# Kernel tuning notes

Hardware: AMD Instinct MI355X
Metric: run time of the kernel (lower is better)

## Reference

```python
import jax, jax.numpy as jnp
import numpy as np

B, NQ, NKV = 2, 2048, 2048
DIM, CTX_DIM = 1024, 1024
HEADS, DIM_HEAD = 16, 64
INNER = HEADS * DIM_HEAD  # 1024
SCALE = DIM_HEAD ** -0.5


def setup_inputs() -> dict:
    key = jax.random.key(0)
    ks = jax.random.split(key, 6)
    x = jax.random.normal(ks[0], (B, NQ, DIM), dtype=jnp.float32)
    context = jax.random.normal(ks[1], (B, NKV, CTX_DIM), dtype=jnp.float32)
    # nn.Linear weights stored as [out, in] in torch; we keep [in, out] for x @ W.
    Wq = jax.random.normal(ks[2], (DIM, INNER), dtype=jnp.float32) / np.sqrt(DIM)
    Wkv = jax.random.normal(ks[3], (CTX_DIM, 2 * INNER), dtype=jnp.float32) / np.sqrt(CTX_DIM)
    Wout = jax.random.normal(ks[4], (INNER, DIM), dtype=jnp.float32) / np.sqrt(INNER)
    bout = jax.random.normal(ks[5], (DIM,), dtype=jnp.float32) * 0.01
    return {"x": x, "context": context, "Wq": Wq, "Wkv": Wkv, "Wout": Wout, "bout": bout}


def reference(x, context, Wq, Wkv, Wout, bout):
    q = x @ Wq                      # [B, Nq, inner]
    kv = context @ Wkv              # [B, Nkv, 2*inner]
    k, v = jnp.split(kv, 2, axis=-1)

    def split_heads(t):             # [B, N, inner] -> [B, H, N, dh]
        return t.reshape(t.shape[0], t.shape[1], HEADS, DIM_HEAD).transpose(0, 2, 1, 3)

    q, k, v = split_heads(q), split_heads(k), split_heads(v)
    dots = jnp.einsum('bhqd,bhkd->bhqk', q, k) * SCALE  # [B, H, Nq, Nkv]
    attn = jax.nn.softmax(dots, axis=-1)
    out = jnp.einsum('bhqk,bhkd->bhqd', attn, v)        # [B, H, Nq, dh]
    out = out.transpose(0, 2, 1, 3).reshape(out.shape[0], out.shape[2], INNER)
    return out @ Wout + bout        # [B, Nq, dim]
```

## Files before the change

kernel.cpp:

```cpp
#include <hip/hip_runtime.h>
#include <hip/hip_bf16.h>
#include <stdint.h>

#define NQ 2048
#define NKV 2048
#define DIM 1024
#define INNER 1024
#define HEADS 16
#define DH 64
#define BATCH 2

typedef float f32x4 __attribute__((ext_vector_type(4)));
typedef __bf16 bf16x8 __attribute__((ext_vector_type(8)));
typedef unsigned int u32x4 __attribute__((ext_vector_type(4)));

__device__ inline ushort f2b(float f) {
    uint32_t u = __builtin_bit_cast(uint32_t, f);
    u += 0x7fff + ((u >> 16) & 1);
    return (ushort)(u >> 16);
}

__device__ inline uint pkbf16(float lo, float hi) {
    __hip_bfloat162 h = __float22bfloat162_rn(make_float2(lo, hi));
    uint r;
    __builtin_memcpy(&r, &h, 4);
    return r;
}

__device__ __forceinline__ void gload16(const void* g, void* lds) {
    __builtin_amdgcn_global_load_lds(
        (const __attribute__((address_space(1))) unsigned int*)g,
        (__attribute__((address_space(3))) unsigned int*)lds, 16, 0, 0);
}

__global__ void prep(const float* __restrict__ x, const float* __restrict__ ctx,
                     const float* __restrict__ Wq, const float* __restrict__ Wkv,
                     const float* __restrict__ Wout,
                     ushort* __restrict__ xb, ushort* __restrict__ cb,
                     ushort* __restrict__ Wqt, ushort* __restrict__ Wkvt,
                     ushort* __restrict__ Woutt) {
    int z = blockIdx.z;
    if (z < 4) {
        __shared__ ushort tile[32][33];
        const float* src; ushort* dst; int C;
        if (z == 0)      { src = Wq;          dst = Wqt;                C = 1024; }
        else if (z == 1) { src = Wkv;         dst = Wkvt;               C = 2048; }
        else if (z == 2) { src = Wkv + 1024;  dst = Wkvt + 1024 * 1024; C = 2048; }
        else             { src = Wout;        dst = Woutt;              C = 1024; }
        int c0 = blockIdx.x * 32, r0 = blockIdx.y * 32;
        int tx = threadIdx.x, ty = threadIdx.y;
#pragma unroll
        for (int i = 0; i < 4; i++)
            tile[ty + i * 8][tx] = f2b(src[(size_t)(r0 + ty + i * 8) * C + c0 + tx]);
        __syncthreads();
#pragma unroll
        for (int i = 0; i < 4; i++)
            dst[(size_t)(c0 + ty + i * 8) * 1024 + r0 + tx] = tile[tx][ty + i * 8];
    } else {
        const int n4 = (BATCH * NQ * DIM) / 4;
        int fb = blockIdx.y * 32 + blockIdx.x;
        int t = threadIdx.y * 32 + threadIdx.x;
        for (int i = fb * 256 + t; i < 2 * n4; i += 1024 * 256) {
            float4 v;
            if (i < n4) v = ((const float4*)x)[i];
            else        v = ((const float4*)ctx)[i - n4];
            ushort4 o;
            o.x = f2b(v.x); o.y = f2b(v.y); o.z = f2b(v.z); o.w = f2b(v.w);
            if (i < n4) ((ushort4*)xb)[i] = o;
            else        ((ushort4*)cb)[i - n4] = o;
        }
    }
}

__global__ __launch_bounds__(256) void gemm_qkv(const ushort* __restrict__ xb, const ushort* __restrict__ cb,
                                                const ushort* __restrict__ Wqt, const ushort* __restrict__ Wkvt,
                                                ushort* __restrict__ qb, ushort* __restrict__ kb,
                                                ushort* __restrict__ vtb, float qscale) {
    constexpr int K = 1024, NT = 32;
    __shared__ ushort lds[24576];
    int flat = blockIdx.x;
    int swz = (flat & 7) * 96 + (flat >> 3);
    bool isq = swz < 256;
    const ushort *A, *Bt;
    int m0, n0;
    if (isq) { A = xb; Bt = Wqt;  m0 = (swz >> 3) * 128;  n0 = (swz & 7) * 128; }
    else     { int b2 = swz - 256; A = cb; Bt = Wkvt; m0 = (b2 >> 4) * 128; n0 = (b2 & 15) * 128; }
    int t = threadIdx.x, l = t & 63, w = t >> 6;
    int wr = w >> 1, wc = w & 1;
    int lg = l >> 4, lc = l & 15;
    f32x4 acc[4][4] = {};

    auto stage = [&](int buf, int k0) {
#pragma unroll
        for (int i = 0; i < 2; i++) {
            int s = w + i * 4;
            gload16(A + (size_t)(m0 + (s & 1) * 64 + l) * K + k0 + (s >> 1) * 8, &lds[buf * 8192 + s * 512]);
            gload16(Bt + (size_t)(n0 + (s & 1) * 64 + l) * K + k0 + (s >> 1) * 8, &lds[buf * 8192 + 4096 + s * 512]);
        }
    };

    stage(0, 0);
    stage(1, 32);
    for (int tt = 0; tt < NT; ++tt) {
        int cur = tt % 3;
        if (tt + 2 < NT) {
            stage((tt + 2) % 3, (tt + 2) * 32);
            asm volatile("s_waitcnt vmcnt(8)" ::: "memory");
        } else if (tt + 1 < NT) {
            asm volatile("s_waitcnt vmcnt(4)" ::: "memory");
        } else {
            asm volatile("s_waitcnt vmcnt(0)" ::: "memory");
        }
        __builtin_amdgcn_s_barrier();
        asm volatile("" ::: "memory");
        bf16x8 af[4], bf[4];
#pragma unroll
        for (int mi = 0; mi < 4; mi++)
            af[mi] = *(const bf16x8*)&lds[cur * 8192 + (lg * 128 + wr * 64 + mi * 16 + lc) * 8];
#pragma unroll
        for (int ni = 0; ni < 4; ni++)
            bf[ni] = *(const bf16x8*)&lds[cur * 8192 + 4096 + (lg * 128 + wc * 64 + ni * 16 + lc) * 8];
        __builtin_amdgcn_s_setprio(1);
#pragma unroll
        for (int mi = 0; mi < 4; mi++)
#pragma unroll
            for (int ni = 0; ni < 4; ni++)
                acc[mi][ni] = __builtin_amdgcn_mfma_f32_16x16x32_bf16(af[mi], bf[ni], acc[mi][ni], 0, 0, 0);
        __builtin_amdgcn_s_setprio(0);
        asm volatile("s_waitcnt lgkmcnt(0)" ::: "memory");
        __builtin_amdgcn_s_barrier();
        asm volatile("" ::: "memory");
    }
    if (isq) {
#pragma unroll
        for (int mi = 0; mi < 4; mi++)
#pragma unroll
            for (int ni = 0; ni < 4; ni++)
#pragma unroll
                for (int r = 0; r < 4; r++) {
                    int m = m0 + wr * 64 + mi * 16 + lg * 4 + r;
                    int n = n0 + wc * 64 + ni * 16 + lc;
                    qb[(size_t)m * 1024 + n] = f2b(acc[mi][ni][r] * qscale);
                }
    } else if (n0 < 1024) {
#pragma unroll
        for (int mi = 0; mi < 4; mi++)
#pragma unroll
            for (int ni = 0; ni < 4; ni++)
#pragma unroll
                for (int r = 0; r < 4; r++) {
                    int m = m0 + wr * 64 + mi * 16 + lg * 4 + r;
                    int n = n0 + wc * 64 + ni * 16 + lc;
                    kb[(size_t)m * 1024 + n] = f2b(acc[mi][ni][r]);
                }
    } else {
        int b = m0 >> 11, kv0 = m0 & 2047;
        int h0 = (n0 - 1024) >> 6;
#pragma unroll
        for (int mi = 0; mi < 4; mi++)
#pragma unroll
            for (int ni = 0; ni < 4; ni++)
#pragma unroll
                for (int r = 0; r < 4; r++) {
                    int ml = wr * 64 + mi * 16 + lg * 4 + r;
                    int nl = wc * 64 + ni * 16 + lc;
                    lds[nl * 136 + ml] = f2b(acc[mi][ni][r]);
                }
        __syncthreads();
#pragma unroll
        for (int c = 0; c < 8; c++) {
            int idx = c * 256 + t;
            int rrow = idx >> 4;
            int chunk = idx & 15;
            int h = h0 + (rrow >> 6), d = rrow & 63;
            u32x4 v = *(u32x4*)&lds[rrow * 136 + chunk * 8];
            *(u32x4*)&vtb[(((size_t)b * HEADS + h) * DH + d) * (size_t)NKV + kv0 + chunk * 8] = v;
        }
    }
}

__global__ __launch_bounds__(256) void gemm_out(const ushort* __restrict__ A, const ushort* __restrict__ Bt,
                                                float* __restrict__ C0, const float* __restrict__ bias) {
    constexpr int K = 1024, NT = 32;
    __shared__ ushort lds[24576];
    int flat = blockIdx.x;
    int swz = (flat & 7) * 32 + (flat >> 3);
    int m0 = (swz >> 3) * 128, n0 = (swz & 7) * 128;
    int t = threadIdx.x, l = t & 63, w = t >> 6;
    int wr = w >> 1, wc = w & 1;
    int lg = l >> 4, lc = l & 15;
    f32x4 acc[4][4] = {};

    auto stage = [&](int buf, int k0) {
#pragma unroll
        for (int i = 0; i < 2; i++) {
            int s = w + i * 4;
            gload16(A + (size_t)(m0 + (s & 1) * 64 + l) * K + k0 + (s >> 1) * 8, &lds[buf * 8192 + s * 512]);
            gload16(Bt + (size_t)(n0 + (s & 1) * 64 + l) * K + k0 + (s >> 1) * 8, &lds[buf * 8192 + 4096 + s * 512]);
        }
    };

    stage(0, 0);
    stage(1, 32);
    for (int tt = 0; tt < NT; ++tt) {
        int cur = tt % 3;
        if (tt + 2 < NT) {
            stage((tt + 2) % 3, (tt + 2) * 32);
            asm volatile("s_waitcnt vmcnt(8)" ::: "memory");
        } else if (tt + 1 < NT) {
            asm volatile("s_waitcnt vmcnt(4)" ::: "memory");
        } else {
            asm volatile("s_waitcnt vmcnt(0)" ::: "memory");
        }
        __builtin_amdgcn_s_barrier();
        asm volatile("" ::: "memory");
        bf16x8 af[4], bf[4];
#pragma unroll
        for (int mi = 0; mi < 4; mi++)
            af[mi] = *(const bf16x8*)&lds[cur * 8192 + (lg * 128 + wr * 64 + mi * 16 + lc) * 8];
#pragma unroll
        for (int ni = 0; ni < 4; ni++)
            bf[ni] = *(const bf16x8*)&lds[cur * 8192 + 4096 + (lg * 128 + wc * 64 + ni * 16 + lc) * 8];
        __builtin_amdgcn_s_setprio(1);
#pragma unroll
        for (int mi = 0; mi < 4; mi++)
#pragma unroll
            for (int ni = 0; ni < 4; ni++)
                acc[mi][ni] = __builtin_amdgcn_mfma_f32_16x16x32_bf16(af[mi], bf[ni], acc[mi][ni], 0, 0, 0);
        __builtin_amdgcn_s_setprio(0);
        asm volatile("s_waitcnt lgkmcnt(0)" ::: "memory");
        __builtin_amdgcn_s_barrier();
        asm volatile("" ::: "memory");
    }
#pragma unroll
    for (int mi = 0; mi < 4; mi++)
#pragma unroll
        for (int ni = 0; ni < 4; ni++)
#pragma unroll
            for (int r = 0; r < 4; r++) {
                int m = m0 + wr * 64 + mi * 16 + lg * 4 + r;
                int n = n0 + wc * 64 + ni * 16 + lc;
                C0[(size_t)m * 1024 + n] = acc[mi][ni][r] + bias[n];
            }
}

__global__ __launch_bounds__(256, 3) void attn3(const ushort* __restrict__ qb, const ushort* __restrict__ kb,
                                                const ushort* __restrict__ vtb, ushort* __restrict__ ob) {
    __shared__ ushort Qs[8 * 128 * 8];
    __shared__ ushort Ks[2][4096];
    __shared__ ushort Vs[2][4096];
    int flat = blockIdx.x;
    int swz = (flat & 7) * 64 + (flat >> 3);
    int qt = swz & 15, h = (swz >> 4) & 15, b = swz >> 8;
    int t = threadIdx.x, l = t & 63, w = t >> 6;
    int lg = l >> 4, lc = l & 15;
    int xsw = (lc << 1) & 0x1C;
    const ushort* Qg = qb + (size_t)b * NQ * INNER + h * DH;
    const ushort* Kg = kb + (size_t)b * NKV * INNER + h * DH;
    const ushort* Vg = vtb + (((size_t)b * HEADS + h) * DH) * NKV;
    int q0 = qt * 128;

#pragma unroll
    for (int i = 0; i < 4; i++) {
        int s = w * 4 + i;
        gload16(Qg + (size_t)(q0 + (s & 1) * 64 + l) * INNER + (s >> 1) * 8, &Qs[s * 512]);
    }
    auto stageKV = [&](int buf, int kv0) {
#pragma unroll
        for (int i = 0; i < 2; i++) {
            int s = w + i * 4;
            gload16(Kg + (size_t)(kv0 + l) * INNER + s * 8, &Ks[buf][s * 512]);
            gload16(Vg + (size_t)l * NKV + kv0 + s * 8, &Vs[buf][s * 512]);
        }
    };
    stageKV(0, 0);
    __syncthreads();

    bf16x8 qf[2][2];
#pragma unroll
    for (int mi = 0; mi < 2; mi++)
#pragma unroll
        for (int kc = 0; kc < 2; kc++)
            qf[mi][kc] = *(const bf16x8*)&Qs[((kc * 4 + lg) * 128 + w * 32 + mi * 16 + lc) * 8];
    __syncthreads();

    uint* Ps = (uint*)Qs + w * 1024;
    f32x4 o[2][4] = {};
    float m_[2] = {-1e30f, -1e30f}, s_[2] = {0.f, 0.f};

    for (int tt = 0; tt < NKV / 64; ++tt) {
        int cur = tt & 1;
        if (tt + 1 < NKV / 64) stageKV(cur ^ 1, (tt + 1) * 64);
        f32x4 st[2][4] = {};
        __builtin_amdgcn_s_setprio(1);
#pragma unroll
        for (int kc = 0; kc < 2; kc++)
#pragma unroll
            for (int nb = 0; nb < 4; nb++) {
                bf16x8 kf = *(const bf16x8*)&Ks[cur][((kc * 4 + lg) * 64 + nb * 16 + lc) * 8];
                st[0][nb] = __builtin_amdgcn_mfma_f32_16x16x32_bf16(kf, qf[0][kc], st[0][nb], 0, 0, 0);
                st[1][nb] = __builtin_amdgcn_mfma_f32_16x16x32_bf16(kf, qf[1][kc], st[1][nb], 0, 0, 0);
            }
        __builtin_amdgcn_s_setprio(0);
#pragma unroll
        for (int mi = 0; mi < 2; mi++) {
            float mx = st[mi][0][0];
#pragma unroll
            for (int nb = 0; nb < 4; nb++)
#pragma unroll
                for (int r = 0; r < 4; r++) mx = fmaxf(mx, st[mi][nb][r]);
            mx = fmaxf(mx, __shfl_xor(mx, 16));
            mx = fmaxf(mx, __shfl_xor(mx, 32));
            if (!__all(mx - m_[mi] <= 8.f)) {
                float mn = fmaxf(m_[mi], mx);
                float fac = __builtin_amdgcn_exp2f(m_[mi] - mn);
                m_[mi] = mn;
                s_[mi] *= fac;
#pragma unroll
                for (int nb = 0; nb < 4; nb++) o[mi][nb] *= fac;
            }
            float mn = m_[mi];
            float rs = 0.f;
#pragma unroll
            for (int nb = 0; nb < 4; nb++) {
                float p0 = __builtin_amdgcn_exp2f(st[mi][nb][0] - mn);
                float p1 = __builtin_amdgcn_exp2f(st[mi][nb][1] - mn);
                float p2 = __builtin_amdgcn_exp2f(st[mi][nb][2] - mn);
                float p3 = __builtin_amdgcn_exp2f(st[mi][nb][3] - mn);
                rs += (p0 + p1) + (p2 + p3);
                uint2 pw;
                pw.x = pkbf16(p0, p1);
                pw.y = pkbf16(p2, p3);
                *(uint2*)&Ps[(mi * 16 + lc) * 32 + ((nb * 8 + lg * 2) ^ xsw)] = pw;
            }
            rs += __shfl_xor(rs, 16);
            rs += __shfl_xor(rs, 32);
            s_[mi] += rs;
        }
        asm volatile("" ::: "memory");
        bf16x8 pf[2][2], vf[4][2];
#pragma unroll
        for (int mi = 0; mi < 2; mi++)
#pragma unroll
            for (int kc = 0; kc < 2; kc++)
                pf[mi][kc] = *(const bf16x8*)&Ps[(mi * 16 + lc) * 32 + ((kc * 16 + lg * 4) ^ xsw)];
#pragma unroll
        for (int nb = 0; nb < 4; nb++)
#pragma unroll
            for (int kc = 0; kc < 2; kc++)
                vf[nb][kc] = *(const bf16x8*)&Vs[cur][((kc * 4 + lg) * 64 + nb * 16 + lc) * 8];
        __builtin_amdgcn_s_setprio(1);
#pragma unroll
        for (int nb = 0; nb < 4; nb++)
#pragma unroll
            for (int kc = 0; kc < 2; kc++) {
                o[0][nb] = __builtin_amdgcn_mfma_f32_16x16x32_bf16(vf[nb][kc], pf[0][kc], o[0][nb], 0, 0, 0);
                o[1][nb] = __builtin_amdgcn_mfma_f32_16x16x32_bf16(vf[nb][kc], pf[1][kc], o[1][nb], 0, 0, 0);
            }
        __builtin_amdgcn_s_setprio(0);
        __syncthreads();
    }
    ushort* Og = ob + (size_t)b * NQ * INNER + h * DH;
#pragma unroll
    for (int mi = 0; mi < 2; mi++) {
        float inv = 1.f / s_[mi];
        int q = q0 + w * 32 + mi * 16 + lc;
#pragma unroll
        for (int nb = 0; nb < 4; nb++) {
            uint2 pw;
            pw.x = pkbf16(o[mi][nb][0] * inv, o[mi][nb][1] * inv);
            pw.y = pkbf16(o[mi][nb][2] * inv, o[mi][nb][3] * inv);
            *(uint2*)&Og[(size_t)q * INNER + nb * 16 + lg * 4] = pw;
        }
    }
}

extern "C" void kernel_launch(void* const* d_in, const int* in_sizes, int n_in,
                              void* d_out, int out_size, void* d_ws, size_t ws_size,
                              hipStream_t stream) {
    const float* x    = (const float*)d_in[0];
    const float* ctx  = (const float*)d_in[1];
    const float* Wq   = (const float*)d_in[2];
    const float* Wkv  = (const float*)d_in[3];
    const float* Wout = (const float*)d_in[4];
    const float* bout = (const float*)d_in[5];
    float* out = (float*)d_out;

    if (ws_size < (size_t)(56u << 20)) return;
    char* ws = (char*)d_ws;
    ushort* xb    = (ushort*)(ws);
    ushort* cb    = (ushort*)(ws + (8u << 20));
    ushort* ob    = (ushort*)(ws + (8u << 20));
    ushort* qb    = (ushort*)(ws + (16u << 20));
    ushort* kb    = (ushort*)(ws + (24u << 20));
    ushort* vtb   = (ushort*)(ws + (32u << 20));
    ushort* Wqt   = (ushort*)(ws + (48u << 20));
    ushort* Wkvt  = (ushort*)(ws + (50u << 20));
    ushort* Woutt = (ushort*)(ws + (54u << 20));

    prep<<<dim3(32, 32, 5), dim3(32, 8), 0, stream>>>(x, ctx, Wq, Wkv, Wout, xb, cb, Wqt, Wkvt, Woutt);
    gemm_qkv<<<768, 256, 0, stream>>>(xb, cb, Wqt, Wkvt, qb, kb, vtb, 0.125f * 1.44269504f);
    attn3<<<512, 256, 0, stream>>>(qb, kb, vtb, ob);
    gemm_out<<<256, 256, 0, stream>>>(ob, Woutt, out, bout);
}
```

Measured before the change: 166.0 us.

## Load K/V fragments directly from global into registers, drop LDS staging

The attention kernel no longer stages Q, K and V tiles through shared memory with double buffering and block barriers. Each wave now loads its MFMA fragments straight from global memory, prefetching the next K tile into a ping-pong register set, and loads V per iteration. This removes the __syncthreads and LDS traffic, but each of the four waves now fetches the same K/V data separately, multiplying global/L2 traffic. Register pressure also rises, and launch bounds are relaxed from 3 to 2 blocks per CU.

After: 217.4 us. 31.0% more time.

```diff
diff --git a/kernel.cpp b/kernel.cpp
--- a/kernel.cpp
+++ b/kernel.cpp
@@ -244,11 +244,9 @@
             }
 }
 
-__global__ __launch_bounds__(256, 3) void attn3(const ushort* __restrict__ qb, const ushort* __restrict__ kb,
+__global__ __launch_bounds__(256, 2) void attn4(const ushort* __restrict__ qb, const ushort* __restrict__ kb,
                                                 const ushort* __restrict__ vtb, ushort* __restrict__ ob) {
-    __shared__ ushort Qs[8 * 128 * 8];
-    __shared__ ushort Ks[2][4096];
-    __shared__ ushort Vs[2][4096];
+    __shared__ uint Ps_all[4][1024];
     int flat = blockIdx.x;
     int swz = (flat & 7) * 64 + (flat >> 3);
     int qt = swz & 15, h = (swz >> 4) & 15, b = swz >> 8;
@@ -260,46 +258,47 @@
     const ushort* Vg = vtb + (((size_t)b * HEADS + h) * DH) * NKV;
     int q0 = qt * 128;
 
-#pragma unroll
-    for (int i = 0; i < 4; i++) {
-        int s = w * 4 + i;
-        gload16(Qg + (size_t)(q0 + (s & 1) * 64 + l) * INNER + (s >> 1) * 8, &Qs[s * 512]);
-    }
-    auto stageKV = [&](int buf, int kv0) {
-#pragma unroll
-        for (int i = 0; i < 2; i++) {
-            int s = w + i * 4;
-            gload16(Kg + (size_t)(kv0 + l) * INNER + s * 8, &Ks[buf][s * 512]);
-            gload16(Vg + (size_t)l * NKV + kv0 + s * 8, &Vs[buf][s * 512]);
-        }
-    };
-    stageKV(0, 0);
-    __syncthreads();
-
     bf16x8 qf[2][2];
 #pragma unroll
     for (int mi = 0; mi < 2; mi++)
 #pragma unroll
         for (int kc = 0; kc < 2; kc++)
-            qf[mi][kc] = *(const bf16x8*)&Qs[((kc * 4 + lg) * 128 + w * 32 + mi * 16 + lc) * 8];
-    __syncthreads();
-
-    uint* Ps = (uint*)Qs + w * 1024;
+            qf[mi][kc] = *(const bf16x8*)&Qg[(size_t)(q0 + w * 32 + mi * 16 + lc) * INNER + (kc * 4 + lg) * 8];
+
+    uint* Ps = Ps_all[w];
     f32x4 o[2][4] = {};
     float m_[2] = {-1e30f, -1e30f}, s_[2] = {0.f, 0.f};
 
-    for (int tt = 0; tt < NKV / 64; ++tt) {
-        int cur = tt & 1;
-        if (tt + 1 < NKV / 64) stageKV(cur ^ 1, (tt + 1) * 64);
+    bf16x8 kfA[2][4], kfB[2][4];
+#pragma unroll
+    for (int kc = 0; kc < 2; kc++)
+#pragma unroll
+        for (int nb = 0; nb < 4; nb++)
+            kfA[kc][nb] = *(const bf16x8*)&Kg[(size_t)(nb * 16 + lc) * INNER + (kc * 4 + lg) * 8];
+
+    auto body = [&](bf16x8 (&kcur)[2][4], bf16x8 (&knxt)[2][4], int tt) {
+        int kv0 = tt * 64;
+        if (tt + 1 < NKV / 64) {
+#pragma unroll
+            for (int kc = 0; kc < 2; kc++)
+#pragma unroll
+                for (int nb = 0; nb < 4; nb++)
+                    knxt[kc][nb] = *(const bf16x8*)&Kg[(size_t)(kv0 + 64 + nb * 16 + lc) * INNER + (kc * 4 + lg) * 8];
+        }
+        bf16x8 vf[4][2];
+#pragma unroll
+        for (int nb = 0; nb < 4; nb++)
+#pragma unroll
+            for (int kc = 0; kc < 2; kc++)
+                vf[nb][kc] = *(const bf16x8*)&Vg[(size_t)(nb * 16 + lc) * NKV + kv0 + (kc * 4 + lg) * 8];
         f32x4 st[2][4] = {};
         __builtin_amdgcn_s_setprio(1);
 #pragma unroll
         for (int kc = 0; kc < 2; kc++)
 #pragma unroll
             for (int nb = 0; nb < 4; nb++) {
-                bf16x8 kf = *(const bf16x8*)&Ks[cur][((kc * 4 + lg) * 64 + nb * 16 + lc) * 8];
-                st[0][nb] = __builtin_amdgcn_mfma_f32_16x16x32_bf16(kf, qf[0][kc], st[0][nb], 0, 0, 0);
-                st[1][nb] = __builtin_amdgcn_mfma_f32_16x16x32_bf16(kf, qf[1][kc], st[1][nb], 0, 0, 0);
+                st[0][nb] = __builtin_amdgcn_mfma_f32_16x16x32_bf16(kcur[kc][nb], qf[0][kc], st[0][nb], 0, 0, 0);
+                st[1][nb] = __builtin_amdgcn_mfma_f32_16x16x32_bf16(kcur[kc][nb], qf[1][kc], st[1][nb], 0, 0, 0);
             }
         __builtin_amdgcn_s_setprio(0);
 #pragma unroll
@@ -338,17 +337,12 @@
             s_[mi] += rs;
         }
         asm volatile("" ::: "memory");
-        bf16x8 pf[2][2], vf[4][2];
+        bf16x8 pf[2][2];
 #pragma unroll
         for (int mi = 0; mi < 2; mi++)
 #pragma unroll
             for (int kc = 0; kc < 2; kc++)
                 pf[mi][kc] = *(const bf16x8*)&Ps[(mi * 16 + lc) * 32 + ((kc * 16 + lg * 4) ^ xsw)];
-#pragma unroll
-        for (int nb = 0; nb < 4; nb++)
-#pragma unroll
-            for (int kc = 0; kc < 2; kc++)
-                vf[nb][kc] = *(const bf16x8*)&Vs[cur][((kc * 4 + lg) * 64 + nb * 16 + lc) * 8];
         __builtin_amdgcn_s_setprio(1);
 #pragma unroll
         for (int nb = 0; nb < 4; nb++)
@@ -358,8 +352,13 @@
                 o[1][nb] = __builtin_amdgcn_mfma_f32_16x16x32_bf16(vf[nb][kc], pf[1][kc], o[1][nb], 0, 0, 0);
             }
         __builtin_amdgcn_s_setprio(0);
-        __syncthreads();
-    }
+    };
+
+    for (int tt = 0; tt < NKV / 64; tt += 2) {
+        body(kfA, kfB, tt);
+        body(kfB, kfA, tt + 1);
+    }
+
     ushort* Og = ob + (size_t)b * NQ * INNER + h * DH;
 #pragma unroll
     for (int mi = 0; mi < 2; mi++) {
@@ -400,6 +399,6 @@
 
     prep<<<dim3(32, 32, 5), dim3(32, 8), 0, stream>>>(x, ctx, Wq, Wkv, Wout, xb, cb, Wqt, Wkvt, Woutt);
     gemm_qkv<<<768, 256, 0, stream>>>(xb, cb, Wqt, Wkvt, qb, kb, vtb, 0.125f * 1.44269504f);
-    attn3<<<512, 256, 0, stream>>>(qb, kb, vtb, ob);
+    attn4<<<512, 256, 0, stream>>>(qb, kb, vtb, ob);
     gemm_out<<<256, 256, 0, stream>>>(ob, Woutt, out, bout);
 }
```

## Split attention over KV halves and merge partials in a combine kernel

Applied to the files above, without the earlier changes.

Splits each attention block's KV range into two halves, doubling the grid from 512 to 1024 blocks so each block loops over half the tiles. Each half writes normalized bf16 partial outputs plus per-row max and sum stats, and a new combine kernel reweights and merges the two partials into the final attention output. The aim is better CU occupancy and load balance on the 256-CU device, where 512 blocks at 3 per CU leaves many slots idle. It costs an extra kernel launch, extra global traffic for the partials, and an extra bf16 rounding of the intermediate outputs.

After: 173.9 us. 4.8% more time.

```diff
diff --git a/kernel.cpp b/kernel.cpp
--- a/kernel.cpp
+++ b/kernel.cpp
@@ -13,11 +13,16 @@
 typedef float f32x4 __attribute__((ext_vector_type(4)));
 typedef __bf16 bf16x8 __attribute__((ext_vector_type(8)));
 typedef unsigned int u32x4 __attribute__((ext_vector_type(4)));
+typedef ushort us8 __attribute__((ext_vector_type(8)));
 
 __device__ inline ushort f2b(float f) {
     uint32_t u = __builtin_bit_cast(uint32_t, f);
     u += 0x7fff + ((u >> 16) & 1);
     return (ushort)(u >> 16);
+}
+
+__device__ inline float b2f(ushort u) {
+    return __builtin_bit_cast(float, (uint32_t)u << 16);
 }
 
 __device__ inline uint pkbf16(float lo, float hi) {
@@ -244,21 +249,26 @@
             }
 }
 
-__global__ __launch_bounds__(256, 3) void attn3(const ushort* __restrict__ qb, const ushort* __restrict__ kb,
-                                                const ushort* __restrict__ vtb, ushort* __restrict__ ob) {
+__global__ __launch_bounds__(256, 3) void attn5(const ushort* __restrict__ qb, const ushort* __restrict__ kb,
+                                                const ushort* __restrict__ vtb,
+                                                ushort* __restrict__ O0, ushort* __restrict__ O1,
+                                                float2* __restrict__ st0, float2* __restrict__ st1) {
     __shared__ ushort Qs[8 * 128 * 8];
     __shared__ ushort Ks[2][4096];
     __shared__ ushort Vs[2][4096];
     int flat = blockIdx.x;
-    int swz = (flat & 7) * 64 + (flat >> 3);
-    int qt = swz & 15, h = (swz >> 4) & 15, b = swz >> 8;
+    int swz = (flat & 7) * 128 + (flat >> 3);
+    int qt = swz & 15, h = (swz >> 4) & 15, b = (swz >> 8) & 1, split = swz >> 9;
     int t = threadIdx.x, l = t & 63, w = t >> 6;
     int lg = l >> 4, lc = l & 15;
     int xsw = (lc << 1) & 0x1C;
     const ushort* Qg = qb + (size_t)b * NQ * INNER + h * DH;
     const ushort* Kg = kb + (size_t)b * NKV * INNER + h * DH;
     const ushort* Vg = vtb + (((size_t)b * HEADS + h) * DH) * NKV;
+    ushort* Op = split ? O1 : O0;
+    float2* stp = split ? st1 : st0;
     int q0 = qt * 128;
+    int kv_base = split * (NKV / 2);
 
 #pragma unroll
     for (int i = 0; i < 4; i++) {
@@ -269,8 +279,8 @@
 #pragma unroll
         for (int i = 0; i < 2; i++) {
             int s = w + i * 4;
-            gload16(Kg + (size_t)(kv0 + l) * INNER + s * 8, &Ks[buf][s * 512]);
-            gload16(Vg + (size_t)l * NKV + kv0 + s * 8, &Vs[buf][s * 512]);
+            gload16(Kg + (size_t)(kv_base + kv0 + l) * INNER + s * 8, &Ks[buf][s * 512]);
+            gload16(Vg + (size_t)l * NKV + kv_base + kv0 + s * 8, &Vs[buf][s * 512]);
         }
     };
     stageKV(0, 0);
@@ -288,9 +298,10 @@
     f32x4 o[2][4] = {};
     float m_[2] = {-1e30f, -1e30f}, s_[2] = {0.f, 0.f};
 
-    for (int tt = 0; tt < NKV / 64; ++tt) {
+    constexpr int NTILES = (NKV / 2) / 64;
+    for (int tt = 0; tt < NTILES; ++tt) {
         int cur = tt & 1;
-        if (tt + 1 < NKV / 64) stageKV(cur ^ 1, (tt + 1) * 64);
+        if (tt + 1 < NTILES) stageKV(cur ^ 1, (tt + 1) * 64);
         f32x4 st[2][4] = {};
         __builtin_amdgcn_s_setprio(1);
 #pragma unroll
@@ -360,7 +371,7 @@
         __builtin_amdgcn_s_setprio(0);
         __syncthreads();
     }
-    ushort* Og = ob + (size_t)b * NQ * INNER + h * DH;
+    ushort* Og = Op + (size_t)b * NQ * INNER + h * DH;
 #pragma unroll
     for (int mi = 0; mi < 2; mi++) {
         float inv = 1.f / s_[mi];
@@ -372,7 +383,43 @@
             pw.y = pkbf16(o[mi][nb][2] * inv, o[mi][nb][3] * inv);
             *(uint2*)&Og[(size_t)q * INNER + nb * 16 + lg * 4] = pw;
         }
-    }
+        if (lg == 0) {
+            float2 v; v.x = m_[mi]; v.y = s_[mi];
+            stp[(((size_t)b * HEADS + h) << 11) + q] = v;
+        }
+    }
+}
+
+__global__ __launch_bounds__(256) void combine(const ushort* __restrict__ O0, const ushort* __restrict__ O1,
+                                               const float2* __restrict__ st0, const float2* __restrict__ st1,
+                                               ushort* __restrict__ ob) {
+    int idx = blockIdx.x * 256 + threadIdx.x;
+    int row = idx >> 3, c = idx & 7;
+    int b = row >> 15, rem = row & 32767;
+    int q = rem >> 4, h = rem & 15;
+    int sidx = (((b * HEADS + h)) << 11) + q;
+    float2 a = st0[sidx], bb = st1[sidx];
+    float ms = fmaxf(a.x, bb.x);
+    float w0 = a.y * __builtin_amdgcn_exp2f(a.x - ms);
+    float w1 = bb.y * __builtin_amdgcn_exp2f(bb.x - ms);
+    float inv = 1.f / (w0 + w1);
+    w0 *= inv; w1 *= inv;
+    size_t off = ((size_t)(b * NQ + q)) * INNER + h * DH + c * 8;
+    us8 v0 = *(const us8*)&O0[off];
+    us8 v1 = *(const us8*)&O1[off];
+    uint2 r0, r1;
+    float f0 = w0 * b2f(v0[0]) + w1 * b2f(v1[0]);
+    float f1 = w0 * b2f(v0[1]) + w1 * b2f(v1[1]);
+    float f2 = w0 * b2f(v0[2]) + w1 * b2f(v1[2]);
+    float f3 = w0 * b2f(v0[3]) + w1 * b2f(v1[3]);
+    float f4 = w0 * b2f(v0[4]) + w1 * b2f(v1[4]);
+    float f5 = w0 * b2f(v0[5]) + w1 * b2f(v1[5]);
+    float f6 = w0 * b2f(v0[6]) + w1 * b2f(v1[6]);
+    float f7 = w0 * b2f(v0[7]) + w1 * b2f(v1[7]);
+    r0.x = pkbf16(f0, f1); r0.y = pkbf16(f2, f3);
+    r1.x = pkbf16(f4, f5); r1.y = pkbf16(f6, f7);
+    u32x4 pk = {r0.x, r0.y, r1.x, r1.y};
+    *(u32x4*)&ob[off] = pk;
 }
 
 extern "C" void kernel_launch(void* const* d_in, const int* in_sizes, int n_in,
@@ -389,17 +436,22 @@
     if (ws_size < (size_t)(56u << 20)) return;
     char* ws = (char*)d_ws;
     ushort* xb    = (ushort*)(ws);
+    ushort* Op1   = (ushort*)(ws);
     ushort* cb    = (ushort*)(ws + (8u << 20));
-    ushort* ob    = (ushort*)(ws + (8u << 20));
+    ushort* Op0   = (ushort*)(ws + (8u << 20));
     ushort* qb    = (ushort*)(ws + (16u << 20));
+    ushort* ob    = (ushort*)(ws + (16u << 20));
     ushort* kb    = (ushort*)(ws + (24u << 20));
     ushort* vtb   = (ushort*)(ws + (32u << 20));
+    float2* st0   = (float2*)(ws + (40u << 20));
+    float2* st1   = (float2*)(ws + (41u << 20));
     ushort* Wqt   = (ushort*)(ws + (48u << 20));
     ushort* Wkvt  = (ushort*)(ws + (50u << 20));
     ushort* Woutt = (ushort*)(ws + (54u << 20));
 
     prep<<<dim3(32, 32, 5), dim3(32, 8), 0, stream>>>(x, ctx, Wq, Wkv, Wout, xb, cb, Wqt, Wkvt, Woutt);
     gemm_qkv<<<768, 256, 0, stream>>>(xb, cb, Wqt, Wkvt, qb, kb, vtb, 0.125f * 1.44269504f);
-    attn3<<<512, 256, 0, stream>>>(qb, kb, vtb, ob);
+    attn5<<<1024, 256, 0, stream>>>(qb, kb, vtb, Op0, Op1, st0, st1);
+    combine<<<2048, 256, 0, stream>>>(Op0, Op1, st0, st1, ob);
     gemm_out<<<256, 256, 0, stream>>>(ob, Woutt, out, bout);
 }
```

## Switch attention to 32x32 MFMA with register-resident P and triple-buffered KV

Applied to the files above, without the earlier changes.

Rewrites the attention inner loop to use 32x32x16 bf16 MFMAs, so each wave holds one 32-query row block. The P matrix is rearranged in registers with v_permlane32_swap instead of being written to and read back from LDS. K/V staging is triple-buffered with explicit vmcnt waits and a single barrier per iteration, replacing the double-buffer plus trailing __syncthreads. The aims are fewer LDS round trips, less sync overhead and higher MFMA efficiency. In exchange, LDS use rises, launch bounds drop to 2 blocks per CU, and the fine-grained vmcnt accounting is easy to get wrong.

Measured after the change: 160.9 us (median of 2 runs). 1.03x faster.

```diff
diff --git a/kernel.cpp b/kernel.cpp
--- a/kernel.cpp
+++ b/kernel.cpp
@@ -11,6 +11,7 @@
 #define BATCH 2
 
 typedef float f32x4 __attribute__((ext_vector_type(4)));
+typedef float f32x16 __attribute__((ext_vector_type(16)));
 typedef __bf16 bf16x8 __attribute__((ext_vector_type(8)));
 typedef unsigned int u32x4 __attribute__((ext_vector_type(4)));
 
@@ -244,17 +245,16 @@
             }
 }
 
-__global__ __launch_bounds__(256, 3) void attn3(const ushort* __restrict__ qb, const ushort* __restrict__ kb,
+__global__ __launch_bounds__(256, 2) void attn6(const ushort* __restrict__ qb, const ushort* __restrict__ kb,
                                                 const ushort* __restrict__ vtb, ushort* __restrict__ ob) {
-    __shared__ ushort Qs[8 * 128 * 8];
-    __shared__ ushort Ks[2][4096];
-    __shared__ ushort Vs[2][4096];
+    __shared__ ushort Qs[8192];
+    __shared__ ushort Ks[3][4096];
+    __shared__ ushort Vs[3][4096];
     int flat = blockIdx.x;
     int swz = (flat & 7) * 64 + (flat >> 3);
     int qt = swz & 15, h = (swz >> 4) & 15, b = swz >> 8;
     int t = threadIdx.x, l = t & 63, w = t >> 6;
-    int lg = l >> 4, lc = l & 15;
-    int xsw = (lc << 1) & 0x1C;
+    int ll = l & 31, hi = l >> 5;
     const ushort* Qg = qb + (size_t)b * NQ * INNER + h * DH;
     const ushort* Kg = kb + (size_t)b * NKV * INNER + h * DH;
     const ushort* Vg = vtb + (((size_t)b * HEADS + h) * DH) * NKV;
@@ -274,104 +274,111 @@
         }
     };
     stageKV(0, 0);
-    __syncthreads();
-
-    bf16x8 qf[2][2];
-#pragma unroll
-    for (int mi = 0; mi < 2; mi++)
-#pragma unroll
-        for (int kc = 0; kc < 2; kc++)
-            qf[mi][kc] = *(const bf16x8*)&Qs[((kc * 4 + lg) * 128 + w * 32 + mi * 16 + lc) * 8];
-    __syncthreads();
-
-    uint* Ps = (uint*)Qs + w * 1024;
-    f32x4 o[2][4] = {};
-    float m_[2] = {-1e30f, -1e30f}, s_[2] = {0.f, 0.f};
-
-    for (int tt = 0; tt < NKV / 64; ++tt) {
-        int cur = tt & 1;
-        if (tt + 1 < NKV / 64) stageKV(cur ^ 1, (tt + 1) * 64);
-        f32x4 st[2][4] = {};
+    stageKV(1, 64);
+    asm volatile("s_waitcnt vmcnt(8)" ::: "memory");
+    __builtin_amdgcn_s_barrier();
+    asm volatile("" ::: "memory");
+
+    bf16x8 qf[4];
+#pragma unroll
+    for (int dchunk = 0; dchunk < 4; dchunk++) {
+        int dc = dchunk * 2 + hi;
+        qf[dchunk] = *(const bf16x8*)&Qs[(dc * 128 + w * 32 + ll) * 8];
+    }
+
+    f32x16 o0 = {}, o1 = {};
+    float m_ = -1e30f, s_ = 0.f;
+
+    constexpr int NT2 = NKV / 64;
+    for (int tt = 0; tt < NT2; ++tt) {
+        int cur = tt % 3;
+        if (tt + 1 < NT2) {
+            asm volatile("s_waitcnt vmcnt(4)" ::: "memory");
+        } else {
+            asm volatile("s_waitcnt vmcnt(0)" ::: "memory");
+        }
+        __builtin_amdgcn_s_barrier();
+        asm volatile("" ::: "memory");
+        if (tt + 2 < NT2) stageKV((tt + 2) % 3, (tt + 2) * 64);
+
+        f32x16 st0 = {}, st1 = {};
         __builtin_amdgcn_s_setprio(1);
 #pragma unroll
-        for (int kc = 0; kc < 2; kc++)
-#pragma unroll
-            for (int nb = 0; nb < 4; nb++) {
-                bf16x8 kf = *(const bf16x8*)&Ks[cur][((kc * 4 + lg) * 64 + nb * 16 + lc) * 8];
-                st[0][nb] = __builtin_amdgcn_mfma_f32_16x16x32_bf16(kf, qf[0][kc], st[0][nb], 0, 0, 0);
-                st[1][nb] = __builtin_amdgcn_mfma_f32_16x16x32_bf16(kf, qf[1][kc], st[1][nb], 0, 0, 0);
+        for (int dchunk = 0; dchunk < 4; dchunk++) {
+            int dc = dchunk * 2 + hi;
+            bf16x8 kf0 = *(const bf16x8*)&Ks[cur][(dc * 64 + ll) * 8];
+            bf16x8 kf1 = *(const bf16x8*)&Ks[cur][(dc * 64 + 32 + ll) * 8];
+            st0 = __builtin_amdgcn_mfma_f32_32x32x16_bf16(kf0, qf[dchunk], st0, 0, 0, 0);
+            st1 = __builtin_amdgcn_mfma_f32_32x32x16_bf16(kf1, qf[dchunk], st1, 0, 0, 0);
+        }
+        __builtin_amdgcn_s_setprio(0);
+
+        float mx = st0[0];
+#pragma unroll
+        for (int r = 1; r < 16; r++) mx = fmaxf(mx, st0[r]);
+#pragma unroll
+        for (int r = 0; r < 16; r++) mx = fmaxf(mx, st1[r]);
+        mx = fmaxf(mx, __shfl_xor(mx, 32));
+        if (!__all(mx - m_ <= 8.f)) {
+            float mn = fmaxf(m_, mx);
+            float fac = __builtin_amdgcn_exp2f(m_ - mn);
+            m_ = mn;
+            s_ *= fac;
+            o0 *= fac;
+            o1 *= fac;
+        }
+        float mn = m_;
+        float pp[32];
+        float rs = 0.f;
+#pragma unroll
+        for (int r = 0; r < 16; r++) { pp[r] = __builtin_amdgcn_exp2f(st0[r] - mn); rs += pp[r]; }
+#pragma unroll
+        for (int r = 0; r < 16; r++) { pp[16 + r] = __builtin_amdgcn_exp2f(st1[r] - mn); rs += pp[16 + r]; }
+        rs += __shfl_xor(rs, 32);
+        s_ += rs;
+
+        bf16x8 pb[4];
+#pragma unroll
+        for (int kvb = 0; kvb < 2; kvb++)
+#pragma unroll
+            for (int c = 0; c < 2; c++) {
+                int base = kvb * 16 + c * 8;
+                uint a0 = pkbf16(pp[base + 0], pp[base + 1]);
+                uint a1 = pkbf16(pp[base + 2], pp[base + 3]);
+                uint b0 = pkbf16(pp[base + 4], pp[base + 5]);
+                uint b1 = pkbf16(pp[base + 6], pp[base + 7]);
+                asm volatile("v_permlane32_swap_b32 %0, %1" : "+v"(a0), "+v"(b0));
+                asm volatile("v_permlane32_swap_b32 %0, %1" : "+v"(a1), "+v"(b1));
+                u32x4 wrd = {a0, a1, b0, b1};
+                pb[kvb * 2 + c] = __builtin_bit_cast(bf16x8, wrd);
             }
+
+        __builtin_amdgcn_s_setprio(1);
+#pragma unroll
+        for (int kvchunk = 0; kvchunk < 4; kvchunk++) {
+            int kvc = kvchunk * 2 + hi;
+            bf16x8 vf0 = *(const bf16x8*)&Vs[cur][(kvc * 64 + ll) * 8];
+            bf16x8 vf1 = *(const bf16x8*)&Vs[cur][(kvc * 64 + 32 + ll) * 8];
+            o0 = __builtin_amdgcn_mfma_f32_32x32x16_bf16(vf0, pb[kvchunk], o0, 0, 0, 0);
+            o1 = __builtin_amdgcn_mfma_f32_32x32x16_bf16(vf1, pb[kvchunk], o1, 0, 0, 0);
+        }
         __builtin_amdgcn_s_setprio(0);
-#pragma unroll
-        for (int mi = 0; mi < 2; mi++) {
-            float mx = st[mi][0][0];
-#pragma unroll
-            for (int nb = 0; nb < 4; nb++)
-#pragma unroll
-                for (int r = 0; r < 4; r++) mx = fmaxf(mx, st[mi][nb][r]);
-            mx = fmaxf(mx, __shfl_xor(mx, 16));
-            mx = fmaxf(mx, __shfl_xor(mx, 32));
-            if (!__all(mx - m_[mi] <= 8.f)) {
-                float mn = fmaxf(m_[mi], mx);
-                float fac = __builtin_amdgcn_exp2f(m_[mi] - mn);
-                m_[mi] = mn;
-                s_[mi] *= fac;
-#pragma unroll
-                for (int nb = 0; nb < 4; nb++) o[mi][nb] *= fac;
-            }
-            float mn = m_[mi];
-            float rs = 0.f;
-#pragma unroll
-            for (int nb = 0; nb < 4; nb++) {
-                float p0 = __builtin_amdgcn_exp2f(st[mi][nb][0] - mn);
-                float p1 = __builtin_amdgcn_exp2f(st[mi][nb][1] - mn);
-                float p2 = __builtin_amdgcn_exp2f(st[mi][nb][2] - mn);
-                float p3 = __builtin_amdgcn_exp2f(st[mi][nb][3] - mn);
-                rs += (p0 + p1) + (p2 + p3);
-                uint2 pw;
-                pw.x = pkbf16(p0, p1);
-                pw.y = pkbf16(p2, p3);
-                *(uint2*)&Ps[(mi * 16 + lc) * 32 + ((nb * 8 + lg * 2) ^ xsw)] = pw;
-            }
-            rs += __shfl_xor(rs, 16);
-            rs += __shfl_xor(rs, 32);
-            s_[mi] += rs;
-        }
-        asm volatile("" ::: "memory");
-        bf16x8 pf[2][2], vf[4][2];
-#pragma unroll
-        for (int mi = 0; mi < 2; mi++)
-#pragma unroll
-            for (int kc = 0; kc < 2; kc++)
-                pf[mi][kc] = *(const bf16x8*)&Ps[(mi * 16 + lc) * 32 + ((kc * 16 + lg * 4) ^ xsw)];
-#pragma unroll
-        for (int nb = 0; nb < 4; nb++)
-#pragma unroll
-            for (int kc = 0; kc < 2; kc++)
-                vf[nb][kc] = *(const bf16x8*)&Vs[cur][((kc * 4 + lg) * 64 + nb * 16 + lc) * 8];
-        __builtin_amdgcn_s_setprio(1);
-#pragma unroll
-        for (int nb = 0; nb < 4; nb++)
-#pragma unroll
-            for (int kc = 0; kc < 2; kc++) {
-                o[0][nb] = __builtin_amdgcn_mfma_f32_16x16x32_bf16(vf[nb][kc], pf[0][kc], o[0][nb], 0, 0, 0);
-                o[1][nb] = __builtin_amdgcn_mfma_f32_16x16x32_bf16(vf[nb][kc], pf[1][kc], o[1][nb], 0, 0, 0);
-            }
-        __builtin_amdgcn_s_setprio(0);
-        __syncthreads();
-    }
+    }
+
     ushort* Og = ob + (size_t)b * NQ * INNER + h * DH;
-#pragma unroll
-    for (int mi = 0; mi < 2; mi++) {
-        float inv = 1.f / s_[mi];
-        int q = q0 + w * 32 + mi * 16 + lc;
-#pragma unroll
-        for (int nb = 0; nb < 4; nb++) {
-            uint2 pw;
-            pw.x = pkbf16(o[mi][nb][0] * inv, o[mi][nb][1] * inv);
-            pw.y = pkbf16(o[mi][nb][2] * inv, o[mi][nb][3] * inv);
-            *(uint2*)&Og[(size_t)q * INNER + nb * 16 + lg * 4] = pw;
-        }
+    float inv = 1.f / s_;
+    int q = q0 + w * 32 + ll;
+#pragma unroll
+    for (int rq = 0; rq < 4; rq++) {
+        int d0 = 8 * rq + 4 * hi;
+        uint2 pw;
+        pw.x = pkbf16(o0[4 * rq + 0] * inv, o0[4 * rq + 1] * inv);
+        pw.y = pkbf16(o0[4 * rq + 2] * inv, o0[4 * rq + 3] * inv);
+        *(uint2*)&Og[(size_t)q * INNER + d0] = pw;
+        uint2 pw1;
+        pw1.x = pkbf16(o1[4 * rq + 0] * inv, o1[4 * rq + 1] * inv);
+        pw1.y = pkbf16(o1[4 * rq + 2] * inv, o1[4 * rq + 3] * inv);
+        *(uint2*)&Og[(size_t)q * INNER + 32 + d0] = pw1;
     }
 }
 
@@ -400,6 +407,6 @@
 
     prep<<<dim3(32, 32, 5), dim3(32, 8), 0, stream>>>(x, ctx, Wq, Wkv, Wout, xb, cb, Wqt, Wkvt, Woutt);
     gemm_qkv<<<768, 256, 0, stream>>>(xb, cb, Wqt, Wkvt, qb, kb, vtb, 0.125f * 1.44269504f);
-    attn3<<<512, 256, 0, stream>>>(qb, kb, vtb, ob);
+    attn6<<<512, 256, 0, stream>>>(qb, kb, vtb, ob);
     gemm_out<<<256, 256, 0, stream>>>(ob, Woutt, out, bout);
 }
```
